# Performance work log

Hardware: AMD Instinct MI355X
Metric: run time of the kernel (lower is better)

Reference implementation:

```python
import jax, jax.numpy as jnp
import numpy as np


def quantize(weights):
    # per-output-channel threshold alpha = mean |w| over in_features
    alpha = jnp.mean(jnp.abs(weights), axis=1, keepdims=True)  # (out, 1)
    return jnp.where(weights > alpha, 1.0,
                     jnp.where(weights < -alpha, -1.0, 0.0)).astype(weights.dtype)


def setup_inputs() -> dict:
    key = jax.random.key(0)
    k1, k2 = jax.random.split(key)
    B, S, DIN, DOUT = 4, 2048, 4096, 4096
    x = jax.random.normal(k1, (B, S, DIN), dtype=jnp.float32)
    weight = jax.random.normal(k2, (DOUT, DIN), dtype=jnp.float32)
    scale = jnp.ones((DOUT, 1), dtype=jnp.float32)
    bias = jnp.zeros((DOUT,), dtype=jnp.float32)
    return {"x": x, "weight": weight, "scale": scale, "bias": bias}


def reference(x, weight, scale, bias):
    # training-mode path with straight-through estimator
    q = quantize(weight)
    qw = jax.lax.stop_gradient(q) + weight - jax.lax.stop_gradient(weight)
    scaled_weight = qw * scale  # (out, in)
    # F.linear: x @ W^T + b
    out = jnp.einsum('bsi,oi->bso', x, scaled_weight) + bias
    return out
```

## Files before the change

kernel.cpp:

```cpp
#include <hip/hip_runtime.h>
#include <hip/hip_bf16.h>
#include <stdint.h>

#define DIN   4096
#define DOUT  4096
#define MTOT  8192

#define BK    64
#define NKT   (DIN / BK)

typedef int i32x4 __attribute__((ext_vector_type(4)));

__device__ __forceinline__ void glds16(const void* g, void* l) {
  __builtin_amdgcn_global_load_lds(
      (__attribute__((address_space(1))) void*)g,
      (__attribute__((address_space(3))) void*)l, 16, 0, 0);
}

__global__ __launch_bounds__(256) void quant_w(const float* __restrict__ W,
                                               int8_t* __restrict__ QW) {
  const int row = blockIdx.x;
  const int t = threadIdx.x;
  const float* wr = W + (size_t)row * DIN;

  float4 v[4];
  double s = 0.0;
#pragma unroll
  for (int j = 0; j < 4; ++j) {
    v[j] = reinterpret_cast<const float4*>(wr)[j * 256 + t];
    s += (double)fabsf(v[j].x) + (double)fabsf(v[j].y) +
         (double)fabsf(v[j].z) + (double)fabsf(v[j].w);
  }
#pragma unroll
  for (int off = 32; off > 0; off >>= 1) s += __shfl_down(s, off, 64);

  __shared__ double ssum[4];
  __shared__ float salpha;
  if ((t & 63) == 0) ssum[t >> 6] = s;
  __syncthreads();
  if (t == 0) salpha = (float)((ssum[0] + ssum[1] + ssum[2] + ssum[3]) / (double)DIN);
  __syncthreads();
  const float alpha = salpha;

  int* qo = reinterpret_cast<int*>(QW + (size_t)row * DIN);
#pragma unroll
  for (int j = 0; j < 4; ++j) {
    int q0 = v[j].x > alpha ? 1 : (v[j].x < -alpha ? -1 : 0);
    int q1 = v[j].y > alpha ? 1 : (v[j].y < -alpha ? -1 : 0);
    int q2 = v[j].z > alpha ? 1 : (v[j].z < -alpha ? -1 : 0);
    int q3 = v[j].w > alpha ? 1 : (v[j].w < -alpha ? -1 : 0);
    qo[j * 256 + t] =
        (q0 & 0xff) | ((q1 & 0xff) << 8) | ((q2 & 0xff) << 16) | ((q3 & 0xff) << 24);
  }
}

__global__ __launch_bounds__(256) void quant_x(const float* __restrict__ X,
                                               int8_t* __restrict__ XQ,
                                               float* __restrict__ XS) {
  const int row = blockIdx.x;
  const int t = threadIdx.x;
  const float* xr = X + (size_t)row * DIN;

  float4 v[4];
  float mx = 0.f;
#pragma unroll
  for (int j = 0; j < 4; ++j) {
    v[j] = reinterpret_cast<const float4*>(xr)[j * 256 + t];
    mx = fmaxf(mx, fmaxf(fmaxf(fabsf(v[j].x), fabsf(v[j].y)),
                         fmaxf(fabsf(v[j].z), fabsf(v[j].w))));
  }
#pragma unroll
  for (int off = 32; off > 0; off >>= 1) mx = fmaxf(mx, __shfl_down(mx, off, 64));

  __shared__ float smax[4];
  __shared__ float sinv, ssc;
  if ((t & 63) == 0) smax[t >> 6] = mx;
  __syncthreads();
  if (t == 0) {
    float rm = fmaxf(fmaxf(smax[0], smax[1]), fmaxf(smax[2], smax[3]));
    sinv = rm > 0.f ? 127.f / rm : 0.f;
    ssc  = rm > 0.f ? rm / 127.f : 0.f;
  }
  __syncthreads();
  const float inv = sinv;
  if (t == 0) XS[row] = ssc;

  int* qo = reinterpret_cast<int*>(XQ + (size_t)row * DIN);
#pragma unroll
  for (int j = 0; j < 4; ++j) {
    int q0 = (int)rintf(v[j].x * inv);
    int q1 = (int)rintf(v[j].y * inv);
    int q2 = (int)rintf(v[j].z * inv);
    int q3 = (int)rintf(v[j].w * inv);
    qo[j * 256 + t] =
        (q0 & 0xff) | ((q1 & 0xff) << 8) | ((q2 & 0xff) << 16) | ((q3 & 0xff) << 24);
  }
}

__global__ __launch_bounds__(512, 2) void gemm256_i8(
    const int8_t* __restrict__ XQ, const int8_t* __restrict__ QW,
    const float* __restrict__ XS, const float* __restrict__ scale,
    const float* __restrict__ bias, float* __restrict__ out) {
  __shared__ int8_t As[2][16384];
  __shared__ int8_t Bs[2][16384];

  const int t = threadIdx.x;
  const int lane = t & 63;
  const int wid = t >> 6;
  const int wr = wid >> 2, wc = wid & 3;
  const int m0 = blockIdx.x * 256;
  const int n0 = blockIdx.y * 256;

  const int8_t* ag = XQ + (size_t)m0 * DIN;
  const int8_t* bg = QW + (size_t)n0 * DIN;

  i32x4 acc[8][4] = {};
  i32x4 aA[4], aB[4];
  i32x4 b0[2], b1[2];

  const int r = lane & 15, kq = lane >> 4;
  const int srow = t >> 2;
  const int scol = ((t & 3) ^ ((srow >> 1) & 3)) * 16;

#define ISSUE_H(Tt_, q_) do {                                                   \
    const int T_ = (Tt_);                                                       \
    if (T_ < NKT) {                                                             \
      const int q__ = (q_), hf_ = q__ >> 1, bf_ = T_ & 1;                       \
      const int8_t* gb_ = (q__ & 1) ? bg : ag;                                  \
      int8_t* lb_ = (q__ & 1) ? &Bs[bf_][0] : &As[bf_][0];                      \
      glds16(gb_ + (size_t)(hf_ * 128 + srow) * DIN + T_ * 64 + scol,           \
             lb_ + hf_ * 8192 + t * 16);                                        \
    }                                                                           \
  } while (0)

#define READA_TO(dst_, buf_, mh_) do {                                          \
    _Pragma("unroll")                                                           \
    for (int mi = 0; mi < 4; ++mi) {                                            \
      const int row_ = wr * 128 + ((mh_) * 4 + mi) * 16 + r;                    \
      dst_[mi] = *reinterpret_cast<const i32x4*>(                               \
          &As[buf_][row_ * 64 + (kq ^ ((row_ >> 1) & 3)) * 16]);                \
    }                                                                           \
  } while (0)

#define READB_TO(dst_, buf_, nh_) do {                                          \
    _Pragma("unroll")                                                           \
    for (int ni = 0; ni < 2; ++ni) {                                            \
      const int row_ = wc * 64 + ((nh_) * 2 + ni) * 16 + r;                     \
      dst_[ni] = *reinterpret_cast<const i32x4*>(                               \
          &Bs[buf_][row_ * 64 + (kq ^ ((row_ >> 1) & 3)) * 16]);                \
    }                                                                           \
  } while (0)

#define MMA2(mh_, areg_) do {                                                   \
    __builtin_amdgcn_s_setprio(1);                                              \
    _Pragma("unroll")                                                           \
    for (int mi = 0; mi < 4; ++mi) {                                            \
      _Pragma("unroll")                                                         \
      for (int ni = 0; ni < 2; ++ni) {                                          \
        acc[(mh_) * 4 + mi][ni] =                                               \
            __builtin_amdgcn_mfma_i32_16x16x64_i8(                              \
                areg_[mi], b0[ni], acc[(mh_) * 4 + mi][ni], 0, 0, 0);           \
        acc[(mh_) * 4 + mi][2 + ni] =                                           \
            __builtin_amdgcn_mfma_i32_16x16x64_i8(                              \
                areg_[mi], b1[ni], acc[(mh_) * 4 + mi][2 + ni], 0, 0, 0);       \
      }                                                                         \
    }                                                                           \
    __builtin_amdgcn_s_setprio(0);                                              \
  } while (0)

#define BAR() __builtin_amdgcn_s_barrier()

#define TILE(T_, buf_) do {                                                     \
      \
    READA_TO(aA, buf_, 0);                                                      \
    READB_TO(b0, buf_, 0);                                                      \
    READB_TO(b1, buf_, 1);                                                      \
    ISSUE_H((T_) + 1, 0);                                                       \
    ISSUE_H((T_) + 1, 2);                                                       \
    MMA2(0, aA);                                                                \
    BAR();                                                                      \
                          \
    READA_TO(aB, buf_, 1);                                                      \
    ISSUE_H((T_) + 2, 1);                                                       \
    ISSUE_H((T_) + 2, 3);                                                       \
    MMA2(1, aB);                                                                \
    if ((T_) < NKT - 2)                                                         \
      asm volatile("s_waitcnt vmcnt(2)" ::: "memory");                          \
    else                                                                        \
      asm volatile("s_waitcnt vmcnt(0)" ::: "memory");                          \
    BAR();                                                                      \
  } while (0)

  ISSUE_H(0, 0); ISSUE_H(0, 2); ISSUE_H(0, 1); ISSUE_H(0, 3);
  ISSUE_H(1, 1); ISSUE_H(1, 3);
  asm volatile("s_waitcnt vmcnt(2)" ::: "memory");
  __builtin_amdgcn_s_barrier();

  for (int T = 0; T < NKT; T += 2) {
    TILE(T, 0);
    TILE(T + 1, 1);
  }

  const int q4 = lane >> 4;
#pragma unroll
  for (int ni = 0; ni < 4; ++ni) {
    const int col = n0 + wc * 64 + ni * 16 + r;
    const float sc = scale[col];
    const float bs = bias[col];
#pragma unroll
    for (int mi = 0; mi < 8; ++mi) {
      const int row = m0 + wr * 128 + mi * 16 + q4 * 4;
#pragma unroll
      for (int e = 0; e < 4; ++e) {
        const float xs = XS[row + e];
        out[(size_t)(row + e) * DOUT + col] =
            (float)acc[mi][ni][e] * (xs * sc) + bs;
      }
    }
  }
#undef ISSUE_H
#undef READA_TO
#undef READB_TO
#undef MMA2
#undef BAR
#undef TILE
}

extern "C" void kernel_launch(void* const* d_in, const int* in_sizes, int n_in,
                              void* d_out, int out_size, void* d_ws, size_t ws_size,
                              hipStream_t stream) {
  const float* X     = (const float*)d_in[0];
  const float* W     = (const float*)d_in[1];
  const float* scale = (const float*)d_in[2];
  const float* bias  = (const float*)d_in[3];
  float* out = (float*)d_out;

  int8_t* QW = (int8_t*)d_ws;
  int8_t* XQ = (int8_t*)d_ws + (size_t)DOUT * DIN;
  float*  XS = (float*)((int8_t*)d_ws + (size_t)DOUT * DIN + (size_t)MTOT * DIN);

  quant_w<<<DOUT, 256, 0, stream>>>(W, QW);
  quant_x<<<MTOT, 256, 0, stream>>>(X, XQ, XS);
  dim3 grid(MTOT / 256, DOUT / 256);
  gemm256_i8<<<grid, 512, 0, stream>>>(XQ, QW, XS, scale, bias, out);
}
```

Baseline: 205.9 us.

## Shrink int8 GEMM tile to 128x128 with 256-thread blocks

Replaces the 256x256 tile, 512-thread int8 MFMA GEMM with a 128x128 tile, 256-thread kernel that keeps four 64x64 warp tiles and runs more blocks per CU. The pipeline is restructured: A and B loads are issued as separate halves and an explicit lgkmcnt wait is added before the mid-tile barrier. The smaller tile gives more blocks and better load balance across CUs, but lowers data reuse per LDS byte and roughly doubles global traffic for the operands.

```diff
diff --git a/kernel.cpp b/kernel.cpp
--- a/kernel.cpp
+++ b/kernel.cpp
@@ -97,93 +97,90 @@
   }
 }
 
-__global__ __launch_bounds__(512, 2) void gemm256_i8(
+__global__ __launch_bounds__(256, 4) void gemm128_i8(
     const int8_t* __restrict__ XQ, const int8_t* __restrict__ QW,
     const float* __restrict__ XS, const float* __restrict__ scale,
     const float* __restrict__ bias, float* __restrict__ out) {
-  __shared__ int8_t As[2][16384];
-  __shared__ int8_t Bs[2][16384];
+  __shared__ int8_t As[2][8192];
+  __shared__ int8_t Bs[2][8192];
 
   const int t = threadIdx.x;
   const int lane = t & 63;
   const int wid = t >> 6;
-  const int wr = wid >> 2, wc = wid & 3;
-  const int m0 = blockIdx.x * 256;
-  const int n0 = blockIdx.y * 256;
+  const int wr = wid >> 1, wc = wid & 1;
+  const int m0 = blockIdx.x * 128;
+  const int n0 = blockIdx.y * 128;
 
   const int8_t* ag = XQ + (size_t)m0 * DIN;
   const int8_t* bg = QW + (size_t)n0 * DIN;
 
-  i32x4 acc[8][4] = {};
-  i32x4 aA[4], aB[4];
-  i32x4 b0[2], b1[2];
+  i32x4 acc[4][4] = {};
+  i32x4 a[4], b[4];
 
   const int r = lane & 15, kq = lane >> 4;
-  const int srow = t >> 2;
-  const int scol = ((t & 3) ^ ((srow >> 1) & 3)) * 16;
-
-#define ISSUE_H(Tt_, q_) do {                                                   \
+
+#define ISSUE_T(Tt_, isb_) do {                                                 \
     const int T_ = (Tt_);                                                       \
     if (T_ < NKT) {                                                             \
-      const int q__ = (q_), hf_ = q__ >> 1, bf_ = T_ & 1;                       \
-      const int8_t* gb_ = (q__ & 1) ? bg : ag;                                  \
-      int8_t* lb_ = (q__ & 1) ? &Bs[bf_][0] : &As[bf_][0];                      \
-      glds16(gb_ + (size_t)(hf_ * 128 + srow) * DIN + T_ * 64 + scol,           \
-             lb_ + hf_ * 8192 + t * 16);                                        \
-    }                                                                           \
-  } while (0)
-
-#define READA_TO(dst_, buf_, mh_) do {                                          \
+      const int bf_ = T_ & 1;                                                   \
+      const int8_t* gb_ = (isb_) ? bg : ag;                                     \
+      int8_t* lb_ = (isb_) ? &Bs[bf_][0] : &As[bf_][0];                         \
+      _Pragma("unroll")                                                         \
+      for (int i_ = 0; i_ < 2; ++i_) {                                          \
+        const int row_ = i_ * 64 + (t >> 2);                                    \
+        const int scol_ = ((t & 3) ^ ((row_ >> 1) & 3)) * 16;                   \
+        glds16(gb_ + (size_t)row_ * DIN + T_ * 64 + scol_,                      \
+               lb_ + i_ * 4096 + t * 16);                                       \
+      }                                                                         \
+    }                                                                           \
+  } while (0)
+
+#define READA(buf_) do {                                                        \
     _Pragma("unroll")                                                           \
     for (int mi = 0; mi < 4; ++mi) {                                            \
-      const int row_ = wr * 128 + ((mh_) * 4 + mi) * 16 + r;                    \
-      dst_[mi] = *reinterpret_cast<const i32x4*>(                               \
+      const int row_ = wr * 64 + mi * 16 + r;                                   \
+      a[mi] = *reinterpret_cast<const i32x4*>(                                  \
           &As[buf_][row_ * 64 + (kq ^ ((row_ >> 1) & 3)) * 16]);                \
     }                                                                           \
   } while (0)
 
-#define READB_TO(dst_, buf_, nh_) do {                                          \
+#define READB(buf_) do {                                                        \
     _Pragma("unroll")                                                           \
-    for (int ni = 0; ni < 2; ++ni) {                                            \
-      const int row_ = wc * 64 + ((nh_) * 2 + ni) * 16 + r;                     \
-      dst_[ni] = *reinterpret_cast<const i32x4*>(                               \
+    for (int ni = 0; ni < 4; ++ni) {                                            \
+      const int row_ = wc * 64 + ni * 16 + r;                                   \
+      b[ni] = *reinterpret_cast<const i32x4*>(                                  \
           &Bs[buf_][row_ * 64 + (kq ^ ((row_ >> 1) & 3)) * 16]);                \
     }                                                                           \
   } while (0)
 
-#define MMA2(mh_, areg_) do {                                                   \
+#define MMA8(nh_) do {                                                          \
     __builtin_amdgcn_s_setprio(1);                                              \
     _Pragma("unroll")                                                           \
     for (int mi = 0; mi < 4; ++mi) {                                            \
       _Pragma("unroll")                                                         \
       for (int ni = 0; ni < 2; ++ni) {                                          \
-        acc[(mh_) * 4 + mi][ni] =                                               \
+        acc[mi][(nh_) * 2 + ni] =                                               \
             __builtin_amdgcn_mfma_i32_16x16x64_i8(                              \
-                areg_[mi], b0[ni], acc[(mh_) * 4 + mi][ni], 0, 0, 0);           \
-        acc[(mh_) * 4 + mi][2 + ni] =                                           \
-            __builtin_amdgcn_mfma_i32_16x16x64_i8(                              \
-                areg_[mi], b1[ni], acc[(mh_) * 4 + mi][2 + ni], 0, 0, 0);       \
+                a[mi], b[(nh_) * 2 + ni], acc[mi][(nh_) * 2 + ni], 0, 0, 0);    \
       }                                                                         \
     }                                                                           \
     __builtin_amdgcn_s_setprio(0);                                              \
   } while (0)
 
 #define BAR() __builtin_amdgcn_s_barrier()
+#define LGKM0() asm volatile("s_waitcnt lgkmcnt(0)" ::: "memory")
 
 #define TILE(T_, buf_) do {                                                     \
-      \
-    READA_TO(aA, buf_, 0);                                                      \
-    READB_TO(b0, buf_, 0);                                                      \
-    READB_TO(b1, buf_, 1);                                                      \
-    ISSUE_H((T_) + 1, 0);                                                       \
-    ISSUE_H((T_) + 1, 2);                                                       \
-    MMA2(0, aA);                                                                \
+                                                                       \
+    READA(buf_);                                                                \
+    READB(buf_);                                                                \
+    ISSUE_T((T_) + 1, 0);                                                       \
+    MMA8(0);                                                                    \
+    LGKM0();         \
     BAR();                                                                      \
-                          \
-    READA_TO(aB, buf_, 1);                                                      \
-    ISSUE_H((T_) + 2, 1);                                                       \
-    ISSUE_H((T_) + 2, 3);                                                       \
-    MMA2(1, aB);                                                                \
+                                                                       \
+    ISSUE_T((T_) + 2, 1);                                                       \
+    MMA8(1);                                                                    \
     if ((T_) < NKT - 2)                                                         \
       asm volatile("s_waitcnt vmcnt(2)" ::: "memory");                          \
     else                                                                        \
@@ -191,8 +188,7 @@
     BAR();                                                                      \
   } while (0)
 
-  ISSUE_H(0, 0); ISSUE_H(0, 2); ISSUE_H(0, 1); ISSUE_H(0, 3);
-  ISSUE_H(1, 1); ISSUE_H(1, 3);
+  ISSUE_T(0, 0); ISSUE_T(0, 1); ISSUE_T(1, 1);
   asm volatile("s_waitcnt vmcnt(2)" ::: "memory");
   __builtin_amdgcn_s_barrier();
 
@@ -208,8 +204,8 @@
     const float sc = scale[col];
     const float bs = bias[col];
 #pragma unroll
-    for (int mi = 0; mi < 8; ++mi) {
-      const int row = m0 + wr * 128 + mi * 16 + q4 * 4;
+    for (int mi = 0; mi < 4; ++mi) {
+      const int row = m0 + wr * 64 + mi * 16 + q4 * 4;
 #pragma unroll
       for (int e = 0; e < 4; ++e) {
         const float xs = XS[row + e];
@@ -218,11 +214,12 @@
       }
     }
   }
-#undef ISSUE_H
-#undef READA_TO
-#undef READB_TO
-#undef MMA2
+#undef ISSUE_T
+#undef READA
+#undef READB
+#undef MMA8
 #undef BAR
+#undef LGKM0
 #undef TILE
 }
 
@@ -241,6 +238,6 @@
 
   quant_w<<<DOUT, 256, 0, stream>>>(W, QW);
   quant_x<<<MTOT, 256, 0, stream>>>(X, XQ, XS);
-  dim3 grid(MTOT / 256, DOUT / 256);
-  gemm256_i8<<<grid, 512, 0, stream>>>(XQ, QW, XS, scale, bias, out);
-}
+  dim3 grid(MTOT / 128, DOUT / 128);
+  gemm128_i8<<<grid, 256, 0, stream>>>(XQ, QW, XS, scale, bias, out);
+}
```

Result: slower. 225.9 us (+9.7%).
